# Kernel tuning notes

Measured on AMD Instinct MI355X. Metric: run time of the kernel, lower is better.

## Reference

```python
import jax, jax.numpy as jnp
import numpy as np

NUM_HEADS = 12
HEAD_DIM = 64


def _rotate_half(x):
    x1, x2 = jnp.split(x, 2, axis=-1)
    return jnp.concatenate([-x2, x1], axis=-1)


def setup_inputs() -> dict:
    key = jax.random.key(0)
    ks = jax.random.split(key, 5)
    B, S, H = 4, 2048, 768
    x = jax.random.normal(ks[0], (B, S, H), dtype=jnp.float32)
    # rope tables per (batch, position, head_dim)
    pos = jnp.arange(S, dtype=jnp.float32)[:, None]
    inv = 1.0 / (10000.0 ** (jnp.arange(0, HEAD_DIM, 2, dtype=jnp.float32) / HEAD_DIM))
    ang = pos * inv[None, :]  # [S, hd/2]
    ang = jnp.concatenate([ang, ang], axis=-1)  # [S, hd]
    cos = jnp.broadcast_to(jnp.cos(ang)[None], (B, S, HEAD_DIM)).astype(jnp.float32)
    sin = jnp.broadcast_to(jnp.sin(ang)[None], (B, S, HEAD_DIM)).astype(jnp.float32)
    Wqkv = jax.random.normal(ks[1], (3 * H, H), dtype=jnp.float32) * 0.02
    Wo = jax.random.normal(ks[2], (H, H), dtype=jnp.float32) * 0.02
    return {"x": x, "cos": cos, "sin": sin, "Wqkv": Wqkv, "Wo": Wo, "window": 64}


def reference(x, cos, sin, Wqkv, Wo, window):
    B, S, H = x.shape
    nh, hd = NUM_HEADS, HEAD_DIM
    scale = hd ** -0.5
    qkv = jnp.einsum('bsh,oh->bso', x, Wqkv)  # [B,S,3H]
    qkv = qkv.reshape(B, S, 3, nh, hd)
    q = qkv[:, :, 0].transpose(0, 2, 1, 3)  # [B,nh,S,hd]
    k = qkv[:, :, 1].transpose(0, 2, 1, 3)
    v = qkv[:, :, 2].transpose(0, 2, 1, 3)
    # RoPE in float32, cos/sin broadcast over heads: [B,1,S,hd]
    c = cos[:, None].astype(jnp.float32)
    s = sin[:, None].astype(jnp.float32)
    qf, kf = q.astype(jnp.float32), k.astype(jnp.float32)
    q = (qf * c + _rotate_half(qf) * s).astype(q.dtype)
    k = (kf * c + _rotate_half(kf) * s).astype(k.dtype)
    scores = jnp.einsum('bhqd,bhkd->bhqk', q, k) * scale
    idx = jnp.arange(S)
    band = jnp.abs(idx[:, None] - idx[None, :]) <= window  # sliding-window mask
    scores = jnp.where(band[None, None], scores, -jnp.inf)
    probs = jax.nn.softmax(scores, axis=-1)
    y = jnp.einsum('bhqk,bhkd->bhqd', probs, v)  # [B,nh,S,hd]
    y = y.transpose(0, 2, 1, 3).reshape(B, S, H)
    return jnp.einsum('bsh,oh->bso', y, Wo)
```

## Files before the change

### kernel.cpp

```cpp
#include <hip/hip_runtime.h>


typedef __attribute__((ext_vector_type(8))) _Float16 f16x8;
typedef __attribute__((ext_vector_type(4))) float    f32x4;

#define BDIM 4
#define SDIM 2048
#define HDIM 768
#define NH   12
#define HD   64
#define NQKV 2304
#define MROWS 8192

__device__ __forceinline__ void gload16(const void* g, void* l) {
    __builtin_amdgcn_global_load_lds(
        (__attribute__((address_space(1))) void*)(g),
        (__attribute__((address_space(3))) void*)(l),
        16, 0, 0);
}

__global__ __launch_bounds__(256) void cvt_f32_f16(
    const float* __restrict__ src, _Float16* __restrict__ dst, int n8)
{
    int i = blockIdx.x * 256 + threadIdx.x;
    if (i >= n8) return;
    const float4* s4 = (const float4*)src + (long)i * 2;
    float4 a = s4[0], b = s4[1];
    f16x8 o;
    o[0] = (_Float16)a.x; o[1] = (_Float16)a.y;
    o[2] = (_Float16)a.z; o[3] = (_Float16)a.w;
    o[4] = (_Float16)b.x; o[5] = (_Float16)b.y;
    o[6] = (_Float16)b.z; o[7] = (_Float16)b.w;
    *((f16x8*)dst + i) = o;
}

template <int EPI>
__global__ __launch_bounds__(256) void gemm_kernel(
    const _Float16* __restrict__ A,
    const _Float16* __restrict__ Bt,
    float* __restrict__ C,
    const float* __restrict__ cosp,
    const float* __restrict__ sinp,
    _Float16* __restrict__ qh,
    _Float16* __restrict__ kh,
    _Float16* __restrict__ vh,
    int M, int N, int K)
{
    __shared__ __align__(16) _Float16 lsA[2][128 * 32];
    __shared__ __align__(16) _Float16 lsB[2][128 * 32];

    int nTn = N >> 7;
    int nwg = gridDim.x;
    int bid = blockIdx.x;
    int wg = bid;
    if ((nwg & 7) == 0) {
        int cpx = nwg >> 3;
        wg = (bid & 7) * cpx + (bid >> 3);
    }
    int tm = wg / nTn, tn = wg % nTn;
    int m0 = tm << 7, n0 = tn << 7;

    int tid  = threadIdx.x;
    int lane = tid & 63;
    int w    = tid >> 6;
    int wr   = w >> 1, wc = w & 1;
    int l15  = lane & 15, lk = lane >> 4;

    f32x4 acc[4][4] = {};

    int srow = tid >> 2;
    int scol = (tid & 3) << 3;
    const _Float16* ga0 = A  + (long)(m0 + srow) * K + scol;
    const _Float16* gb0 = Bt + (long)(n0 + srow) * K + scol;
    const long gstep = (long)64 * K;
    _Float16* laP[2] = { &lsA[0][tid * 8], &lsA[1][tid * 8] };
    _Float16* lbP[2] = { &lsB[0][tid * 8], &lsB[1][tid * 8] };

    const int NK = K >> 5;

#define STAGE(buf, t) do {                                   \
        const _Float16* ga_ = ga0 + (t) * 32;                \
        const _Float16* gb_ = gb0 + (t) * 32;                \
        gload16(ga_,         laP[buf]);                      \
        gload16(ga_ + gstep, laP[buf] + 2048);               \
        gload16(gb_,         lbP[buf]);                      \
        gload16(gb_ + gstep, lbP[buf] + 2048);               \
    } while (0)

    STAGE(0, 0);
    STAGE(1, 1);
    asm volatile("s_waitcnt vmcnt(4)" ::: "memory");
    __builtin_amdgcn_s_barrier();

    int cur = 0;
    for (int it = 0; it < NK; ++it) {
        f16x8 af[4], bfr[4];
#pragma unroll
        for (int m = 0; m < 4; ++m)
            af[m] = *(const f16x8*)&lsA[cur][(wr * 64 + m * 16 + l15) * 32 + lk * 8];
#pragma unroll
        for (int n = 0; n < 4; ++n)
            bfr[n] = *(const f16x8*)&lsB[cur][(wc * 64 + n * 16 + l15) * 32 + lk * 8];

        asm volatile("s_waitcnt lgkmcnt(0)" ::: "memory");
        __builtin_amdgcn_s_barrier();

        if (it + 2 < NK) STAGE(cur, it + 2);

#pragma unroll
        for (int m = 0; m < 4; ++m)
#pragma unroll
            for (int n = 0; n < 4; ++n)
                acc[m][n] = __builtin_amdgcn_mfma_f32_16x16x32_f16(
                    af[m], bfr[n], acc[m][n], 0, 0, 0);

        if (it + 1 < NK) {
            if (it + 2 < NK)
                asm volatile("s_waitcnt vmcnt(4)" ::: "memory");
            else
                asm volatile("s_waitcnt vmcnt(0)" ::: "memory");
            __builtin_amdgcn_s_barrier();
        }
        cur ^= 1;
    }
#undef STAGE

    if (EPI == 0) {
#pragma unroll
        for (int m = 0; m < 4; ++m)
#pragma unroll
            for (int n = 0; n < 4; ++n)
#pragma unroll
                for (int j = 0; j < 4; ++j) {
                    int gr = m0 + wr * 64 + m * 16 + lk * 4 + j;
                    int gc = n0 + wc * 64 + n * 16 + l15;
                    C[(long)gr * N + gc] = acc[m][n][j];
                }
    } else {
        int ht = (n0 >> 6) + wc;
        int t  = ht / NH;
        int h  = ht - t * NH;
        int b  = m0 >> 11;
        long base_bh = ((long)(b * NH + h)) * SDIM;
#pragma unroll
        for (int m = 0; m < 4; ++m) {
#pragma unroll
            for (int j = 0; j < 4; ++j) {
                int gr = m0 + wr * 64 + m * 16 + lk * 4 + j;
                int s  = gr & (SDIM - 1);
                if (t == 2) {
#pragma unroll
                    for (int n = 0; n < 4; ++n) {
                        int d = n * 16 + l15;
                        vh[(base_bh + s) * HD + d] = (_Float16)acc[m][n][j];
                    }
                } else {
                    float vals[4];
#pragma unroll
                    for (int n = 0; n < 4; ++n) vals[n] = acc[m][n][j];
#pragma unroll
                    for (int n = 0; n < 4; ++n) {
                        int d = n * 16 + l15;
                        float cc = cosp[(long)gr * HD + d];
                        float ss = sinp[(long)gr * HD + d];
                        float pv = (n < 2) ? -vals[n + 2] : vals[n - 2];
                        float o  = vals[n] * cc + pv * ss;
                        long oidx = (base_bh + s) * HD + d;
                        if (t == 0) qh[oidx] = (_Float16)o;
                        else        kh[oidx] = (_Float16)o;
                    }
                }
            }
        }
    }
}

#define SSTR 200
#define PSTR 200
__global__ __launch_bounds__(256) void attn_mfma(
    const _Float16* __restrict__ qh,
    const _Float16* __restrict__ kh,
    const _Float16* __restrict__ vh,
    _Float16* __restrict__ yh)
{
    __shared__ __align__(16) _Float16 lsVT[64 * SSTR];
    __shared__ __align__(16) _Float16 lsP [64 * PSTR];

    int bid = blockIdx.x;
    int qt  = bid & 31;
    int bh  = bid >> 5;
    int q0  = qt << 6;
    int k0  = q0 - 64;
    int tid = threadIdx.x;
    int lane = tid & 63;
    int w = tid >> 6;
    int l15 = lane & 15, lg = lane >> 4;

    const _Float16* Qb = qh + (long)bh * SDIM * HD;
    const _Float16* Kb = kh + (long)bh * SDIM * HD;
    const _Float16* Vb = vh + (long)bh * SDIM * HD;

#pragma unroll
    for (int c = 0; c < 3; ++c) {
        int rk = c * 64 + lane;
        int s  = k0 + rk;
        s = s < 0 ? 0 : (s >= SDIM ? SDIM - 1 : s);
        const f16x8* vr = (const f16x8*)(Vb + (long)s * HD + w * 16);
        f16x8 v0 = vr[0], v1 = vr[1];
#pragma unroll
        for (int e = 0; e < 8; ++e) {
            lsVT[(w * 16 + e)     * SSTR + rk] = v0[e];
            lsVT[(w * 16 + 8 + e) * SSTR + rk] = v1[e];
        }
    }

    int qrow = q0 + w * 16 + l15;
    const f16x8* qp = (const f16x8*)(Qb + (long)qrow * HD + lg * 8);
    f16x8 qa0 = qp[0];
    f16x8 qa1 = qp[4];

    float sums[4] = {0.f, 0.f, 0.f, 0.f};
    int iqb = w * 16 + lg * 4;
#pragma unroll 4
    for (int kt = 0; kt < 12; ++kt) {
        int krow = k0 + kt * 16 + l15;
        int kcl = krow < 0 ? 0 : (krow >= SDIM ? SDIM - 1 : krow);
        const f16x8* kp = (const f16x8*)(Kb + (long)kcl * HD + lg * 8);
        f16x8 kb0 = kp[0], kb1 = kp[4];
        f32x4 acc = {0.f, 0.f, 0.f, 0.f};
        acc = __builtin_amdgcn_mfma_f32_16x16x32_f16(qa0, kb0, acc, 0, 0, 0);
        acc = __builtin_amdgcn_mfma_f32_16x16x32_f16(qa1, kb1, acc, 0, 0, 0);
        int jk = kt * 16 + l15;
        bool kin = (krow >= 0) && (krow < SDIM);
#pragma unroll
        for (int j = 0; j < 4; ++j) {
            int i = iqb + j;
            bool valid = kin && (jk >= i) && (jk <= i + 128);
            float p = valid ? __expf(acc[j] * 0.125f) : 0.f;
            sums[j] += p;
            lsP[(w * 16 + lg * 4 + j) * PSTR + jk] = (_Float16)p;
        }
    }

#pragma unroll
    for (int m = 1; m < 16; m <<= 1) {
#pragma unroll
        for (int j = 0; j < 4; ++j)
            sums[j] += __shfl_xor(sums[j], m, 64);
    }
    float inv[4];
#pragma unroll
    for (int j = 0; j < 4; ++j) inv[j] = 1.f / sums[j];

    __syncthreads();

    f32x4 accy[4] = {};
    const _Float16* prow = &lsP[(w * 16 + l15) * PSTR + lg * 8];
#pragma unroll
    for (int kc = 0; kc < 6; ++kc) {
        f16x8 pa = *(const f16x8*)(prow + kc * 32);
#pragma unroll
        for (int dt = 0; dt < 4; ++dt) {
            f16x8 vb = *(const f16x8*)&lsVT[(dt * 16 + l15) * SSTR + kc * 32 + lg * 8];
            accy[dt] = __builtin_amdgcn_mfma_f32_16x16x32_f16(pa, vb, accy[dt], 0, 0, 0);
        }
    }

    int b = bh / NH, h = bh - (bh / NH) * NH;
    long outbase = ((long)b * SDIM) * HDIM + (long)h * HD;
#pragma unroll
    for (int dt = 0; dt < 4; ++dt) {
#pragma unroll
        for (int j = 0; j < 4; ++j) {
            int srow = q0 + w * 16 + lg * 4 + j;
            yh[outbase + (long)srow * HDIM + dt * 16 + l15] =
                (_Float16)(accy[dt][j] * inv[j]);
        }
    }
}

extern "C" void kernel_launch(void* const* d_in, const int* in_sizes, int n_in,
                              void* d_out, int out_size, void* d_ws, size_t ws_size,
                              hipStream_t stream)
{
    const float* x    = (const float*)d_in[0];
    const float* cosp = (const float*)d_in[1];
    const float* sinp = (const float*)d_in[2];
    const float* Wqkv = (const float*)d_in[3];
    const float* Wo   = (const float*)d_in[4];
    float* out = (float*)d_out;

    char* ws = (char*)d_ws;
    _Float16* xh    = (_Float16*)(ws);
    _Float16* wqkvh = (_Float16*)(ws + 12582912);
    _Float16* woh   = (_Float16*)(ws + 16121856);
    _Float16* qh    = (_Float16*)(ws + 17301504);
    _Float16* kh    = (_Float16*)(ws + 29884416);
    _Float16* vh    = (_Float16*)(ws + 42467328);
    _Float16* yh    = (_Float16*)(ws + 55050240);

    cvt_f32_f16<<<(MROWS * HDIM / 8 + 255) / 256, 256, 0, stream>>>(x, xh, MROWS * HDIM / 8);
    cvt_f32_f16<<<(NQKV * HDIM / 8 + 255) / 256, 256, 0, stream>>>(Wqkv, wqkvh, NQKV * HDIM / 8);
    cvt_f32_f16<<<(HDIM * HDIM / 8 + 255) / 256, 256, 0, stream>>>(Wo, woh, HDIM * HDIM / 8);

    {
        dim3 grid((MROWS / 128) * (NQKV / 128));
        gemm_kernel<1><<<grid, 256, 0, stream>>>(
            xh, wqkvh, nullptr, cosp, sinp, qh, kh, vh, MROWS, NQKV, HDIM);
    }

    {
        dim3 grid(BDIM * NH * (SDIM / 64));
        attn_mfma<<<grid, 256, 0, stream>>>(qh, kh, vh, yh);
    }

    {
        dim3 grid((MROWS / 128) * (HDIM / 128));
        gemm_kernel<0><<<grid, 256, 0, stream>>>(
            yh, woh, out, nullptr, nullptr, nullptr, nullptr, nullptr,
            MROWS, HDIM, HDIM);
    }
}
```

Baseline: 114.6 us.

## Enlarge GEMM tiles to 256 rows with 512-thread eight-wave workgroups

The GEMM kernel is templated on the column-fragment count. It now computes 256x256 tiles for the QKV projection and 256x128 tiles for the output projection, using 8 waves of 512 threads. Staging addresses, wait counts and epilogue indexing are adjusted to match. Larger tiles raise operand reuse per LDS load and per global load. The cost is far fewer workgroups (288 and 192) on a 256-CU part, which risks poor wave balance and idle CUs, plus higher register pressure.

Result: slower. 137.3 us (+19.8%).

```diff
diff --git a/kernel.cpp b/kernel.cpp
--- a/kernel.cpp
+++ b/kernel.cpp
@@ -34,8 +34,8 @@
     *((f16x8*)dst + i) = o;
 }
 
-template <int EPI>
-__global__ __launch_bounds__(256) void gemm_kernel(
+template <int NF, int EPI>
+__global__ __launch_bounds__(512) void gemm_kernel(
     const _Float16* __restrict__ A,
     const _Float16* __restrict__ Bt,
     float* __restrict__ C,
@@ -46,95 +46,99 @@
     _Float16* __restrict__ vh,
     int M, int N, int K)
 {
-    __shared__ __align__(16) _Float16 lsA[2][128 * 32];
-    __shared__ __align__(16) _Float16 lsB[2][128 * 32];
-
-    int nTn = N >> 7;
+    constexpr int BN = NF * 64;
+    __shared__ __align__(16) _Float16 lsA[2][256 * 32];
+    __shared__ __align__(16) _Float16 lsB[2][BN * 32];
+
+    int nTn = N / BN;
     int nwg = gridDim.x;
     int bid = blockIdx.x;
-    int wg = bid;
-    if ((nwg & 7) == 0) {
-        int cpx = nwg >> 3;
-        wg = (bid & 7) * cpx + (bid >> 3);
-    }
+    int cpx = nwg >> 3;
+    int wg  = (bid & 7) * cpx + (bid >> 3);
     int tm = wg / nTn, tn = wg % nTn;
-    int m0 = tm << 7, n0 = tn << 7;
+    int m0 = tm << 8, n0 = tn * BN;
 
     int tid  = threadIdx.x;
     int lane = tid & 63;
     int w    = tid >> 6;
-    int wr   = w >> 1, wc = w & 1;
+    int wr   = w >> 2, wc = w & 3;
     int l15  = lane & 15, lk = lane >> 4;
 
-    f32x4 acc[4][4] = {};
-
-    int srow = tid >> 2;
-    int scol = (tid & 3) << 3;
-    const _Float16* ga0 = A  + (long)(m0 + srow) * K + scol;
-    const _Float16* gb0 = Bt + (long)(n0 + srow) * K + scol;
-    const long gstep = (long)64 * K;
-    _Float16* laP[2] = { &lsA[0][tid * 8], &lsA[1][tid * 8] };
-    _Float16* lbP[2] = { &lsB[0][tid * 8], &lsB[1][tid * 8] };
+    f32x4 acc[8][NF] = {};
+
+    int rstage = w * 16 + (lane >> 2);
+    int cstage = (lane & 3) << 3;
+    const _Float16* gaT = A  + (long)(m0 + rstage) * K + cstage;
+    const _Float16* gbT = Bt + (long)(n0 + rstage) * K + cstage;
+    const long gstep = (long)128 * K;
+    _Float16* la0 = &lsA[0][rstage * 32 + cstage];
+    _Float16* la1 = &lsA[1][rstage * 32 + cstage];
+    _Float16* lb0 = &lsB[0][rstage * 32 + cstage];
+    _Float16* lb1 = &lsB[1][rstage * 32 + cstage];
+
+    auto STAGE = [&](_Float16* la, _Float16* lb, int t) {
+        const _Float16* ga_ = gaT + (long)t * 32;
+        const _Float16* gb_ = gbT + (long)t * 32;
+        gload16(ga_,         la);
+        gload16(ga_ + gstep, la + 4096);
+        gload16(gb_,         lb);
+        if constexpr (NF == 4) gload16(gb_ + gstep, lb + 4096);
+    };
+    auto WAIT_PIPE = [] {
+        if constexpr (NF == 4) asm volatile("s_waitcnt vmcnt(4)" ::: "memory");
+        else                   asm volatile("s_waitcnt vmcnt(3)" ::: "memory");
+    };
 
     const int NK = K >> 5;
 
-#define STAGE(buf, t) do {                                   \
-        const _Float16* ga_ = ga0 + (t) * 32;                \
-        const _Float16* gb_ = gb0 + (t) * 32;                \
-        gload16(ga_,         laP[buf]);                      \
-        gload16(ga_ + gstep, laP[buf] + 2048);               \
-        gload16(gb_,         lbP[buf]);                      \
-        gload16(gb_ + gstep, lbP[buf] + 2048);               \
-    } while (0)
-
-    STAGE(0, 0);
-    STAGE(1, 1);
-    asm volatile("s_waitcnt vmcnt(4)" ::: "memory");
+    STAGE(la0, lb0, 0);
+    STAGE(la1, lb1, 1);
+    WAIT_PIPE();
     __builtin_amdgcn_s_barrier();
 
     int cur = 0;
     for (int it = 0; it < NK; ++it) {
-        f16x8 af[4], bfr[4];
-#pragma unroll
-        for (int m = 0; m < 4; ++m)
-            af[m] = *(const f16x8*)&lsA[cur][(wr * 64 + m * 16 + l15) * 32 + lk * 8];
-#pragma unroll
-        for (int n = 0; n < 4; ++n)
-            bfr[n] = *(const f16x8*)&lsB[cur][(wc * 64 + n * 16 + l15) * 32 + lk * 8];
+        const _Float16* lsAc = lsA[cur];
+        const _Float16* lsBc = lsB[cur];
+        f16x8 af[8], bfr[NF];
+#pragma unroll
+        for (int mf = 0; mf < 8; ++mf)
+            af[mf] = *(const f16x8*)&lsAc[(wr * 128 + mf * 16 + l15) * 32 + lk * 8];
+#pragma unroll
+        for (int nf = 0; nf < NF; ++nf)
+            bfr[nf] = *(const f16x8*)&lsBc[(wc * (NF * 16) + nf * 16 + l15) * 32 + lk * 8];
 
         asm volatile("s_waitcnt lgkmcnt(0)" ::: "memory");
         __builtin_amdgcn_s_barrier();
 
-        if (it + 2 < NK) STAGE(cur, it + 2);
-
-#pragma unroll
-        for (int m = 0; m < 4; ++m)
-#pragma unroll
-            for (int n = 0; n < 4; ++n)
-                acc[m][n] = __builtin_amdgcn_mfma_f32_16x16x32_f16(
-                    af[m], bfr[n], acc[m][n], 0, 0, 0);
+        if (it + 2 < NK)
+            STAGE(cur ? la1 : la0, cur ? lb1 : lb0, it + 2);
+
+#pragma unroll
+        for (int mf = 0; mf < 8; ++mf)
+#pragma unroll
+            for (int nf = 0; nf < NF; ++nf)
+                acc[mf][nf] = __builtin_amdgcn_mfma_f32_16x16x32_f16(
+                    af[mf], bfr[nf], acc[mf][nf], 0, 0, 0);
 
         if (it + 1 < NK) {
-            if (it + 2 < NK)
-                asm volatile("s_waitcnt vmcnt(4)" ::: "memory");
-            else
-                asm volatile("s_waitcnt vmcnt(0)" ::: "memory");
+            if (it + 2 < NK) WAIT_PIPE();
+            else asm volatile("s_waitcnt vmcnt(0)" ::: "memory");
             __builtin_amdgcn_s_barrier();
         }
         cur ^= 1;
     }
-#undef STAGE
-
-    if (EPI == 0) {
-#pragma unroll
-        for (int m = 0; m < 4; ++m)
-#pragma unroll
-            for (int n = 0; n < 4; ++n)
+
+    if constexpr (EPI == 0) {
+#pragma unroll
+        for (int mf = 0; mf < 8; ++mf)
+#pragma unroll
+            for (int nf = 0; nf < NF; ++nf)
 #pragma unroll
                 for (int j = 0; j < 4; ++j) {
-                    int gr = m0 + wr * 64 + m * 16 + lk * 4 + j;
-                    int gc = n0 + wc * 64 + n * 16 + l15;
-                    C[(long)gr * N + gc] = acc[m][n][j];
+                    int gr = m0 + wr * 128 + mf * 16 + lk * 4 + j;
+                    int gc = n0 + wc * (NF * 16) + nf * 16 + l15;
+                    C[(long)gr * N + gc] = acc[mf][nf][j];
                 }
     } else {
         int ht = (n0 >> 6) + wc;
@@ -143,28 +147,28 @@
         int b  = m0 >> 11;
         long base_bh = ((long)(b * NH + h)) * SDIM;
 #pragma unroll
-        for (int m = 0; m < 4; ++m) {
+        for (int mf = 0; mf < 8; ++mf) {
 #pragma unroll
             for (int j = 0; j < 4; ++j) {
-                int gr = m0 + wr * 64 + m * 16 + lk * 4 + j;
+                int gr = m0 + wr * 128 + mf * 16 + lk * 4 + j;
                 int s  = gr & (SDIM - 1);
                 if (t == 2) {
 #pragma unroll
-                    for (int n = 0; n < 4; ++n) {
-                        int d = n * 16 + l15;
-                        vh[(base_bh + s) * HD + d] = (_Float16)acc[m][n][j];
+                    for (int nf = 0; nf < NF; ++nf) {
+                        int d = nf * 16 + l15;
+                        vh[(base_bh + s) * HD + d] = (_Float16)acc[mf][nf][j];
                     }
                 } else {
                     float vals[4];
 #pragma unroll
-                    for (int n = 0; n < 4; ++n) vals[n] = acc[m][n][j];
-#pragma unroll
-                    for (int n = 0; n < 4; ++n) {
-                        int d = n * 16 + l15;
+                    for (int nf = 0; nf < 4; ++nf) vals[nf] = acc[mf][nf % NF][j];
+#pragma unroll
+                    for (int nf = 0; nf < 4; ++nf) {
+                        int d = nf * 16 + l15;
                         float cc = cosp[(long)gr * HD + d];
                         float ss = sinp[(long)gr * HD + d];
-                        float pv = (n < 2) ? -vals[n + 2] : vals[n - 2];
-                        float o  = vals[n] * cc + pv * ss;
+                        float pv = (nf < 2) ? -vals[nf + 2] : vals[nf - 2];
+                        float o  = vals[nf] * cc + pv * ss;
                         long oidx = (base_bh + s) * HD + d;
                         if (t == 0) qh[oidx] = (_Float16)o;
                         else        kh[oidx] = (_Float16)o;
@@ -304,8 +308,8 @@
     cvt_f32_f16<<<(HDIM * HDIM / 8 + 255) / 256, 256, 0, stream>>>(Wo, woh, HDIM * HDIM / 8);
 
     {
-        dim3 grid((MROWS / 128) * (NQKV / 128));
-        gemm_kernel<1><<<grid, 256, 0, stream>>>(
+        dim3 grid((MROWS / 256) * (NQKV / 256));
+        gemm_kernel<4, 1><<<grid, 512, 0, stream>>>(
             xh, wqkvh, nullptr, cosp, sinp, qh, kh, vh, MROWS, NQKV, HDIM);
     }
 
@@ -315,8 +319,8 @@
     }
 
     {
-        dim3 grid((MROWS / 128) * (HDIM / 128));
-        gemm_kernel<0><<<grid, 256, 0, stream>>>(
+        dim3 grid((MROWS / 256) * (HDIM / 128));
+        gemm_kernel<2, 0><<<grid, 512, 0, stream>>>(
             yh, woh, out, nullptr, nullptr, nullptr, nullptr, nullptr,
             MROWS, HDIM, HDIM);
     }
```

## Fuse fp32-to-fp16 conversion of x into QKV GEMM loads with swizzled LDS

Applied to the files above, without the earlier changes.

The QKV GEMM now reads x directly in fp32, converts it to fp16 in registers and writes it into an XOR-swizzled LDS tile with K-step 64. This removes the separate conversion pass over x and its fp16 round-trip through memory. The two weight conversions are merged into one launch. The cost is more register pressure and a synchronous A-operand staging path, with a full vmcnt(0) wait each iteration.

After: 114.7 us. Within noise of the previous version (+0.1%).

```diff
diff --git a/kernel.cpp b/kernel.cpp
--- a/kernel.cpp
+++ b/kernel.cpp
@@ -19,31 +19,203 @@
         16, 0, 0);
 }
 
-__global__ __launch_bounds__(256) void cvt_f32_f16(
-    const float* __restrict__ src, _Float16* __restrict__ dst, int n8)
+__global__ __launch_bounds__(256) void cvt_weights(
+    const float* __restrict__ wqkv, const float* __restrict__ wo,
+    _Float16* __restrict__ dq, _Float16* __restrict__ dwo)
 {
+    const int n1 = NQKV * HDIM / 8;
+    const int n2 = HDIM * HDIM / 8;
     int i = blockIdx.x * 256 + threadIdx.x;
-    if (i >= n8) return;
-    const float4* s4 = (const float4*)src + (long)i * 2;
+    const float* s; _Float16* d; int j;
+    if (i < n1)            { s = wqkv; d = dq;  j = i; }
+    else if (i < n1 + n2)  { s = wo;   d = dwo; j = i - n1; }
+    else return;
+    const float4* s4 = (const float4*)s + (long)j * 2;
     float4 a = s4[0], b = s4[1];
     f16x8 o;
     o[0] = (_Float16)a.x; o[1] = (_Float16)a.y;
     o[2] = (_Float16)a.z; o[3] = (_Float16)a.w;
     o[4] = (_Float16)b.x; o[5] = (_Float16)b.y;
     o[6] = (_Float16)b.z; o[7] = (_Float16)b.w;
-    *((f16x8*)dst + i) = o;
-}
-
-template <int EPI>
-__global__ __launch_bounds__(256) void gemm_kernel(
-    const _Float16* __restrict__ A,
+    *((f16x8*)d + j) = o;
+}
+
+__global__ __launch_bounds__(256) void gemm_qkv(
+    const float* __restrict__ A,
     const _Float16* __restrict__ Bt,
-    float* __restrict__ C,
     const float* __restrict__ cosp,
     const float* __restrict__ sinp,
     _Float16* __restrict__ qh,
     _Float16* __restrict__ kh,
-    _Float16* __restrict__ vh,
+    _Float16* __restrict__ vh)
+{
+    const int K = HDIM;
+    __shared__ __align__(16) _Float16 lsA[2][128 * 64];
+    __shared__ __align__(16) _Float16 lsB[2][128 * 64];
+
+    const int nTn = NQKV >> 7;
+    int nwg = gridDim.x;
+    int bid = blockIdx.x;
+    int cpx = nwg >> 3;
+    int wg  = (bid & 7) * cpx + (bid >> 3);
+    int tm = wg / nTn, tn = wg % nTn;
+    int m0 = tm << 7, n0 = tn << 7;
+
+    int tid  = threadIdx.x;
+    int lane = tid & 63;
+    int w    = tid >> 6;
+    int wr   = w >> 1, wc = w & 1;
+    int l15  = lane & 15, lk = lane >> 4;
+
+    f32x4 acc[4][4] = {};
+
+    int arow = tid >> 3;
+    int ag   = tid & 7;
+    const float* gA = A + (long)(m0 + arow) * K + ag * 8;
+    int awr = arow * 64 + ((ag ^ (arow & 7)) << 3);
+    float4 r0, r1, r2, r3, r4, r5, r6, r7;
+
+    int bg = (tid & 7) ^ ((tid >> 3) & 7);
+    const _Float16* gB = Bt + (long)(n0 + (tid >> 3)) * K + bg * 8;
+
+#define ALOAD(t) do {                                                   \
+        const float* p_ = gA + (t) * 64;                                \
+        r0 = ((const float4*)(p_            ))[0];                      \
+        r1 = ((const float4*)(p_            ))[1];                      \
+        r2 = ((const float4*)(p_ +  32L * K))[0];                       \
+        r3 = ((const float4*)(p_ +  32L * K))[1];                       \
+        r4 = ((const float4*)(p_ +  64L * K))[0];                       \
+        r5 = ((const float4*)(p_ +  64L * K))[1];                       \
+        r6 = ((const float4*)(p_ +  96L * K))[0];                       \
+        r7 = ((const float4*)(p_ +  96L * K))[1];                       \
+    } while (0)
+
+#define CVT8(lo, hi, dst) do {                                          \
+        f16x8 v_;                                                       \
+        v_[0] = (_Float16)(lo).x; v_[1] = (_Float16)(lo).y;             \
+        v_[2] = (_Float16)(lo).z; v_[3] = (_Float16)(lo).w;             \
+        v_[4] = (_Float16)(hi).x; v_[5] = (_Float16)(hi).y;             \
+        v_[6] = (_Float16)(hi).z; v_[7] = (_Float16)(hi).w;             \
+        *(f16x8*)(dst) = v_;                                            \
+    } while (0)
+
+#define AWRITE(buf) do {                                                \
+        CVT8(r0, r1, &lsA[buf][awr]);                                   \
+        CVT8(r2, r3, &lsA[buf][awr + 2048]);                            \
+        CVT8(r4, r5, &lsA[buf][awr + 4096]);                            \
+        CVT8(r6, r7, &lsA[buf][awr + 6144]);                            \
+    } while (0)
+
+#define STAGE_B(buf, t) do {                                            \
+        gload16(gB + (t) * 64,            &lsB[buf][tid * 8]);          \
+        gload16(gB + (t) * 64 + 32L * K,  &lsB[buf][tid * 8 + 2048]);   \
+        gload16(gB + (t) * 64 + 64L * K,  &lsB[buf][tid * 8 + 4096]);   \
+        gload16(gB + (t) * 64 + 96L * K,  &lsB[buf][tid * 8 + 6144]);   \
+    } while (0)
+
+    int xg = l15 & 7;
+#define RD(base, rbase, ks, f) do {                                     \
+        _Pragma("unroll")                                               \
+        for (int mf_ = 0; mf_ < 4; ++mf_) {                             \
+            int row_ = (rbase) + mf_ * 16 + l15;                        \
+            (f)[mf_] = *(const f16x8*)&(base)[row_ * 64 +               \
+                (((((ks) << 2) | lk) ^ xg) << 3)];                      \
+        }                                                               \
+    } while (0)
+
+    const int NT = K >> 6;
+
+    ALOAD(0);
+    STAGE_B(0, 0);
+    asm volatile("s_waitcnt vmcnt(0)" ::: "memory");
+    AWRITE(0);
+    ALOAD(1);
+    STAGE_B(1, 1);
+    asm volatile("s_waitcnt lgkmcnt(0)" ::: "memory");
+    __builtin_amdgcn_s_barrier();
+
+    int cur = 0;
+    for (int t = 0; t < NT; ++t) {
+        int nxt = cur ^ 1;
+        f16x8 af[4], bf[4];
+
+        RD(lsA[cur], wr * 64, 0, af);
+        RD(lsB[cur], wc * 64, 0, bf);
+#pragma unroll
+        for (int mf = 0; mf < 4; ++mf)
+#pragma unroll
+            for (int nf = 0; nf < 4; ++nf)
+                acc[mf][nf] = __builtin_amdgcn_mfma_f32_16x16x32_f16(
+                    af[mf], bf[nf], acc[mf][nf], 0, 0, 0);
+
+        RD(lsA[cur], wr * 64, 1, af);
+        RD(lsB[cur], wc * 64, 1, bf);
+#pragma unroll
+        for (int mf = 0; mf < 4; ++mf)
+#pragma unroll
+            for (int nf = 0; nf < 4; ++nf)
+                acc[mf][nf] = __builtin_amdgcn_mfma_f32_16x16x32_f16(
+                    af[mf], bf[nf], acc[mf][nf], 0, 0, 0);
+
+        if (t + 1 < NT) {
+            asm volatile("s_waitcnt vmcnt(0)" ::: "memory");
+            AWRITE(nxt);
+            asm volatile("s_waitcnt lgkmcnt(0)" ::: "memory");
+            __builtin_amdgcn_s_barrier();
+            if (t + 2 < NT) {
+                ALOAD(t + 2);
+                STAGE_B(cur, t + 2);
+            }
+        }
+        cur = nxt;
+    }
+#undef ALOAD
+#undef CVT8
+#undef AWRITE
+#undef STAGE_B
+#undef RD
+
+    int ht = (n0 >> 6) + wc;
+    int tq = ht / NH;
+    int h  = ht - tq * NH;
+    int b  = m0 >> 11;
+    long base_bh = ((long)(b * NH + h)) * SDIM;
+#pragma unroll
+    for (int mf = 0; mf < 4; ++mf) {
+#pragma unroll
+        for (int j = 0; j < 4; ++j) {
+            int gr = m0 + wr * 64 + mf * 16 + lk * 4 + j;
+            int s  = gr & (SDIM - 1);
+            if (tq == 2) {
+#pragma unroll
+                for (int nf = 0; nf < 4; ++nf) {
+                    int d = nf * 16 + l15;
+                    vh[(base_bh + s) * HD + d] = (_Float16)acc[mf][nf][j];
+                }
+            } else {
+                float vals[4];
+#pragma unroll
+                for (int nf = 0; nf < 4; ++nf) vals[nf] = acc[mf][nf][j];
+#pragma unroll
+                for (int nf = 0; nf < 4; ++nf) {
+                    int d = nf * 16 + l15;
+                    float cc = cosp[(long)gr * HD + d];
+                    float ss = sinp[(long)gr * HD + d];
+                    float pv = (nf < 2) ? -vals[nf + 2] : vals[nf - 2];
+                    float o  = vals[nf] * cc + pv * ss;
+                    long oidx = (base_bh + s) * HD + d;
+                    if (tq == 0) qh[oidx] = (_Float16)o;
+                    else         kh[oidx] = (_Float16)o;
+                }
+            }
+        }
+    }
+}
+
+__global__ __launch_bounds__(256) void gemm_op(
+    const _Float16* __restrict__ A,
+    const _Float16* __restrict__ Bt,
+    float* __restrict__ C,
     int M, int N, int K)
 {
     __shared__ __align__(16) _Float16 lsA[2][128 * 32];
@@ -52,11 +224,8 @@
     int nTn = N >> 7;
     int nwg = gridDim.x;
     int bid = blockIdx.x;
-    int wg = bid;
-    if ((nwg & 7) == 0) {
-        int cpx = nwg >> 3;
-        wg = (bid & 7) * cpx + (bid >> 3);
-    }
+    int cpx = nwg >> 3;
+    int wg  = (bid & 7) * cpx + (bid >> 3);
     int tm = wg / nTn, tn = wg % nTn;
     int m0 = tm << 7, n0 = tn << 7;
 
@@ -125,54 +294,16 @@
     }
 #undef STAGE
 
-    if (EPI == 0) {
-#pragma unroll
-        for (int m = 0; m < 4; ++m)
-#pragma unroll
-            for (int n = 0; n < 4; ++n)
-#pragma unroll
-                for (int j = 0; j < 4; ++j) {
-                    int gr = m0 + wr * 64 + m * 16 + lk * 4 + j;
-                    int gc = n0 + wc * 64 + n * 16 + l15;
-                    C[(long)gr * N + gc] = acc[m][n][j];
-                }
-    } else {
-        int ht = (n0 >> 6) + wc;
-        int t  = ht / NH;
-        int h  = ht - t * NH;
-        int b  = m0 >> 11;
-        long base_bh = ((long)(b * NH + h)) * SDIM;
-#pragma unroll
-        for (int m = 0; m < 4; ++m) {
+#pragma unroll
+    for (int m = 0; m < 4; ++m)
+#pragma unroll
+        for (int n = 0; n < 4; ++n)
 #pragma unroll
             for (int j = 0; j < 4; ++j) {
                 int gr = m0 + wr * 64 + m * 16 + lk * 4 + j;
-                int s  = gr & (SDIM - 1);
-                if (t == 2) {
-#pragma unroll
-                    for (int n = 0; n < 4; ++n) {
-                        int d = n * 16 + l15;
-                        vh[(base_bh + s) * HD + d] = (_Float16)acc[m][n][j];
-                    }
-                } else {
-                    float vals[4];
-#pragma unroll
-                    for (int n = 0; n < 4; ++n) vals[n] = acc[m][n][j];
-#pragma unroll
-                    for (int n = 0; n < 4; ++n) {
-                        int d = n * 16 + l15;
-                        float cc = cosp[(long)gr * HD + d];
-                        float ss = sinp[(long)gr * HD + d];
-                        float pv = (n < 2) ? -vals[n + 2] : vals[n - 2];
-                        float o  = vals[n] * cc + pv * ss;
-                        long oidx = (base_bh + s) * HD + d;
-                        if (t == 0) qh[oidx] = (_Float16)o;
-                        else        kh[oidx] = (_Float16)o;
-                    }
-                }
+                int gc = n0 + wc * 64 + n * 16 + l15;
+                C[(long)gr * N + gc] = acc[m][n][j];
             }
-        }
-    }
 }
 
 #define SSTR 200
@@ -291,22 +422,21 @@
     float* out = (float*)d_out;
 
     char* ws = (char*)d_ws;
-    _Float16* xh    = (_Float16*)(ws);
-    _Float16* wqkvh = (_Float16*)(ws + 12582912);
-    _Float16* woh   = (_Float16*)(ws + 16121856);
-    _Float16* qh    = (_Float16*)(ws + 17301504);
-    _Float16* kh    = (_Float16*)(ws + 29884416);
-    _Float16* vh    = (_Float16*)(ws + 42467328);
-    _Float16* yh    = (_Float16*)(ws + 55050240);
-
-    cvt_f32_f16<<<(MROWS * HDIM / 8 + 255) / 256, 256, 0, stream>>>(x, xh, MROWS * HDIM / 8);
-    cvt_f32_f16<<<(NQKV * HDIM / 8 + 255) / 256, 256, 0, stream>>>(Wqkv, wqkvh, NQKV * HDIM / 8);
-    cvt_f32_f16<<<(HDIM * HDIM / 8 + 255) / 256, 256, 0, stream>>>(Wo, woh, HDIM * HDIM / 8);
+    _Float16* wqkvh = (_Float16*)(ws);
+    _Float16* woh   = (_Float16*)(ws + 3538944);
+    _Float16* qh    = (_Float16*)(ws + 4718592);
+    _Float16* kh    = (_Float16*)(ws + 17301504);
+    _Float16* vh    = (_Float16*)(ws + 29884416);
+    _Float16* yh    = (_Float16*)(ws + 42467328);
+
+    {
+        int nthr = NQKV * HDIM / 8 + HDIM * HDIM / 8;
+        cvt_weights<<<(nthr + 255) / 256, 256, 0, stream>>>(Wqkv, Wo, wqkvh, woh);
+    }
 
     {
         dim3 grid((MROWS / 128) * (NQKV / 128));
-        gemm_kernel<1><<<grid, 256, 0, stream>>>(
-            xh, wqkvh, nullptr, cosp, sinp, qh, kh, vh, MROWS, NQKV, HDIM);
+        gemm_qkv<<<grid, 256, 0, stream>>>(x, wqkvh, cosp, sinp, qh, kh, vh);
     }
 
     {
@@ -316,8 +446,6 @@
 
     {
         dim3 grid((MROWS / 128) * (HDIM / 128));
-        gemm_kernel<0><<<grid, 256, 0, stream>>>(
-            yh, woh, out, nullptr, nullptr, nullptr, nullptr, nullptr,
-            MROWS, HDIM, HDIM);
-    }
-}
+        gemm_op<<<grid, 256, 0, stream>>>(yh, woh, out, MROWS, HDIM, HDIM);
+    }
+}
```
